# Optimization experiments

Measured on AMD Instinct MI355X. Metric: run time of the kernel, lower is better.

## Reference

```python
import jax, jax.numpy as jnp
import numpy as np

B, T, C, H = 8, 2048, 1024, 128

def setup_inputs() -> dict:
    key = jax.random.key(0)
    k1, k2, k3, k4 = jax.random.split(key, 4)
    x = jax.random.normal(k1, (B, T, C), dtype=jnp.float32)
    Wq = jax.random.normal(k2, (C, H), dtype=jnp.float32) * (C ** -0.5)
    Wk = jax.random.normal(k3, (C, H), dtype=jnp.float32) * (C ** -0.5)
    Wv = jax.random.normal(k4, (C, H), dtype=jnp.float32) * (C ** -0.5)
    return {"x": x, "Wq": Wq, "Wk": Wk, "Wv": Wv}

def reference(x, Wq, Wk, Wv):
    # x: [B,T,C]; projections (no bias)
    q = jnp.einsum('btc,ch->bth', x, Wq)
    k = jnp.einsum('btc,ch->bth', x, Wk)
    v = jnp.einsum('btc,ch->bth', x, Wv)
    # NOTE: original module has NO 1/sqrt(head_size) scaling
    scores = jnp.einsum('bth,bsh->bts', q, k)  # [B,T,T]
    t = scores.shape[1]
    causal = jnp.tril(jnp.ones((t, t), dtype=bool))
    scores = jnp.where(causal, scores, -jnp.inf)
    attn = jax.nn.softmax(scores, axis=-1)  # dropout is identity in eval
    out = jnp.einsum('bts,bsh->bth', attn, v)  # [B,T,H]
    return out
```

## Files before the change

kernel.cpp:

```cpp
#include <hip/hip_runtime.h>

typedef __bf16 bf16;
typedef _Float16 f16;
typedef f16 f16x4 __attribute__((ext_vector_type(4)));
typedef f16 f16x8 __attribute__((ext_vector_type(8)));
typedef float f32x4 __attribute__((ext_vector_type(4)));

#define MFMA_FP(a, b, c) __builtin_amdgcn_mfma_f32_16x16x32_f16((a), (b), (c), 0, 0, 0)

static constexpr int Bn = 8, T = 2048, C = 1024, H = 128;
static constexpr int M = Bn * T;

__global__ __launch_bounds__(256) void kwt(const float* __restrict__ Wq,
                                           const float* __restrict__ Wk,
                                           const float* __restrict__ Wv,
                                           f16* __restrict__ wt) {
  __shared__ float tl[32][33];
  const int w = blockIdx.z;
  const float* src = (w == 0) ? Wq : (w == 1) ? Wk : Wv;
  f16* dh = wt + (size_t)w * H * C;
  const int k0 = blockIdx.x * 32, n0 = blockIdx.y * 32;
  const int tx = threadIdx.x & 31, ty = threadIdx.x >> 5;
  for (int i = ty; i < 32; i += 8) tl[i][tx] = src[(size_t)(k0 + i) * H + n0 + tx];
  __syncthreads();
  for (int i = ty; i < 32; i += 8)
    dh[(size_t)(n0 + i) * C + k0 + tx] = (f16)tl[tx][i];
}

__global__ __launch_bounds__(256) void proj_kernel(const float* __restrict__ x,
                                                   const f16* __restrict__ wt,
                                                   f16* __restrict__ qo,
                                                   f16* __restrict__ ko,
                                                   f16* __restrict__ vt) {
  __shared__ __align__(16) f16 As[64 * 64];
  __shared__ __align__(16) f16 Bs[128 * 64];
  const int tid = threadIdx.x;
  const int lane = tid & 63, g = lane >> 4, r16 = lane & 15;
  const int wave = tid >> 6, wr = wave >> 1, wc = wave & 1;
  const int m0 = blockIdx.x * 64;
  const int which = blockIdx.y;
  const f16* wh = wt + (size_t)which * H * C;

  int arow[2], aoff[2], alds[2];
  int brow[4], boff[4], blds[4];
#pragma unroll
  for (int it = 0; it < 2; ++it) {
    const int c = it * 256 + tid, r = c >> 3, p = c & 7;
    arow[it] = r; aoff[it] = ((p ^ (r & 7)) << 3); alds[it] = r * 64 + p * 8;
  }
#pragma unroll
  for (int it = 0; it < 4; ++it) {
    const int c = it * 256 + tid, r = c >> 3, p = c & 7;
    brow[it] = r; boff[it] = ((p ^ (r & 7)) << 3); blds[it] = r * 64 + p * 8;
  }

  f32x4 ra[2][2]; f16x8 rb[4];
#pragma unroll
  for (int it = 0; it < 2; ++it) {
    ra[it][0] = *(const f32x4*)&x[(size_t)(m0 + arow[it]) * C + aoff[it]];
    ra[it][1] = *(const f32x4*)&x[(size_t)(m0 + arow[it]) * C + aoff[it] + 4];
  }
#pragma unroll
  for (int it = 0; it < 4; ++it)
    rb[it] = *(const f16x8*)&wh[(size_t)brow[it] * C + boff[it]];

  f32x4 acc[2][4] = {};

  for (int k0 = 0; k0 < C; k0 += 64) {
    __syncthreads();
#pragma unroll
    for (int it = 0; it < 2; ++it) {
      f16x8 av;
#pragma unroll
      for (int j = 0; j < 4; ++j) { av[j] = (f16)ra[it][0][j]; av[4 + j] = (f16)ra[it][1][j]; }
      *(f16x8*)&As[alds[it]] = av;
    }
#pragma unroll
    for (int it = 0; it < 4; ++it) *(f16x8*)&Bs[blds[it]] = rb[it];
    if (k0 + 64 < C) {
      const int kn = k0 + 64;
#pragma unroll
      for (int it = 0; it < 2; ++it) {
        ra[it][0] = *(const f32x4*)&x[(size_t)(m0 + arow[it]) * C + kn + aoff[it]];
        ra[it][1] = *(const f32x4*)&x[(size_t)(m0 + arow[it]) * C + kn + aoff[it] + 4];
      }
#pragma unroll
      for (int it = 0; it < 4; ++it)
        rb[it] = *(const f16x8*)&wh[(size_t)brow[it] * C + kn + boff[it]];
    }
    __syncthreads();
#pragma unroll
    for (int kb = 0; kb < 2; ++kb) {
      f16x8 af[2], bf[4];
#pragma unroll
      for (int mt = 0; mt < 2; ++mt) {
        const int r = wr * 32 + mt * 16 + r16;
        const int phys = (kb * 4 + g) ^ (r & 7);
        af[mt] = *(const f16x8*)&As[r * 64 + phys * 8];
      }
#pragma unroll
      for (int nt = 0; nt < 4; ++nt) {
        const int r = wc * 64 + nt * 16 + r16;
        const int phys = (kb * 4 + g) ^ (r & 7);
        bf[nt] = *(const f16x8*)&Bs[r * 64 + phys * 8];
      }
#pragma unroll
      for (int mt = 0; mt < 2; ++mt)
#pragma unroll
        for (int nt = 0; nt < 4; ++nt)
          acc[mt][nt] = MFMA_FP(af[mt], bf[nt], acc[mt][nt]);
    }
  }

  if (which < 2) {
    f16* dst = which ? ko : qo;
#pragma unroll
    for (int mt = 0; mt < 2; ++mt)
#pragma unroll
      for (int nt = 0; nt < 4; ++nt) {
        const int mb = m0 + wr * 32 + mt * 16 + g * 4;
        const int col = wc * 64 + nt * 16 + r16;
#pragma unroll
        for (int r = 0; r < 4; ++r)
          dst[(size_t)(mb + r) * H + col] = (f16)acc[mt][nt][r];
      }
  } else {
    const int b = m0 >> 11;
    const int tb0 = m0 & 2047;
    f16* vbase = vt + (size_t)b * H * T;
#pragma unroll
    for (int mt = 0; mt < 2; ++mt)
#pragma unroll
      for (int nt = 0; nt < 4; ++nt) {
        const int tib = tb0 + wr * 32 + mt * 16 + g * 4;
        const int h = wc * 64 + nt * 16 + r16;
        f16x4 pk;
#pragma unroll
        for (int r = 0; r < 4; ++r) pk[r] = (f16)acc[mt][nt][r];
        *(f16x4*)&vbase[(size_t)h * T + tib] = pk;
      }
  }
}

__global__ __launch_bounds__(256, 2) void attn_kernel(const f16* __restrict__ qp,
                                                      const f16* __restrict__ kp,
                                                      const f16* __restrict__ vp,
                                                      float* __restrict__ out,
                                                      f16* __restrict__ oS,
                                                      float* __restrict__ MLs) {
  __shared__ __align__(16) f16 KS[2][64 * 128];
  __shared__ __align__(16) f16 VS[2][128 * 64];
  __shared__ __align__(16) f16 Pl[4][16][72];

  const int tid = threadIdx.x, lane = tid & 63, wave = tid >> 6;
  const int g = lane >> 4, q15 = lane & 15;
  const int x7 = q15 & 7;
  const int bb = blockIdx.x;
  const int b = bb & 7;
  const int t2 = bb >> 3;
  const int qt = 31 - (t2 >> 1);
  const int par = t2 & 1;
  const int q0 = qt * 64;
  const int qrow = q0 + wave * 16 + q15;
  const int task = b * 32 + qt;

  const f16* qb = qp + (size_t)b * T * H;
  const f16* kb = kp + (size_t)b * T * H;
  const f16* vb = vp + (size_t)b * H * T;

  int koff[4], voff[4], lo[4];
#pragma unroll
  for (int i = 0; i < 4; ++i) {
    const int u = wave * 4 + i;
    const int rK = u * 4 + (lane >> 4);
    koff[i] = rK * H + (((lane & 15) ^ (rK & 7)) << 3);
    const int hV = u * 8 + (lane >> 3);
    voff[i] = hV * T + (((lane & 7) ^ (hV & 7)) << 3);
    lo[i] = u * 512 + lane * 8;
  }

  const int n = (qt >= par) ? ((qt - par) >> 1) + 1 : 0;

  f16x8 qf[4];
#pragma unroll
  for (int k4 = 0; k4 < 4; ++k4)
    qf[k4] = *(const f16x8*)&qb[(size_t)qrow * H + k4 * 32 + g * 8];

  f32x4 o[8] = {};
  float mrun = -1e30f, lrun = 0.f;

  f16x8 rk[4], rv[4];
#define LOADT(S0)                                                   \
  _Pragma("unroll")                                                 \
  for (int i = 0; i < 4; ++i) {                                     \
    rk[i] = *(const f16x8*)&kb[(size_t)(S0) * H + koff[i]];         \
    rv[i] = *(const f16x8*)&vb[(size_t)(S0) + voff[i]];             \
  }
#define WRITET(BUF)                                                 \
  _Pragma("unroll")                                                 \
  for (int i = 0; i < 4; ++i) {                                     \
    *(f16x8*)&KS[BUF][lo[i]] = rk[i];                               \
    *(f16x8*)&VS[BUF][lo[i]] = rv[i];                               \
  }

  if (n > 0) {
    LOADT(par * 64);
    WRITET(0);
    if (n > 1) LOADT(par * 64 + 128);

    for (int k = 0; k < n; ++k) {
      const int s0 = par * 64 + k * 128;
      const int cur = k & 1;
      __syncthreads();

      f32x4 sacc[4] = {};
#pragma unroll
      for (int mt = 0; mt < 4; ++mt) {
        const int row = mt * 16 + q15;
#pragma unroll
        for (int k4 = 0; k4 < 4; ++k4) {
          const int pch = (k4 * 4 + g) ^ (row & 7);
          const f16x8 kf = *(const f16x8*)&KS[cur][row * 128 + pch * 8];
          sacc[mt] = MFMA_FP(kf, qf[k4], sacc[mt]);
        }
      }
      if (k == n - 1) {
#pragma unroll
        for (int mt = 0; mt < 4; ++mt)
#pragma unroll
          for (int r = 0; r < 4; ++r)
            if (s0 + mt * 16 + g * 4 + r > qrow) sacc[mt][r] = -1e30f;
      }
      float tmax = -1e30f;
#pragma unroll
      for (int mt = 0; mt < 4; ++mt)
#pragma unroll
        for (int r = 0; r < 4; ++r) tmax = fmaxf(tmax, sacc[mt][r]);
      tmax = fmaxf(tmax, __shfl_xor(tmax, 16));
      tmax = fmaxf(tmax, __shfl_xor(tmax, 32));
      const float mnew = fmaxf(mrun, tmax);
      const float alpha = __expf(mrun - mnew);
      float lt = 0.f;
#pragma unroll
      for (int mt = 0; mt < 4; ++mt) {
        f16x4 pk;
#pragma unroll
        for (int r = 0; r < 4; ++r) {
          const float p = __expf(sacc[mt][r] - mnew);
          lt += p;
          pk[r] = (f16)p;
        }
        *(f16x4*)&Pl[wave][q15][mt * 16 + g * 4] = pk;
      }
      lt += __shfl_xor(lt, 16);
      lt += __shfl_xor(lt, 32);
      lrun = lrun * alpha + lt;
      mrun = mnew;
#pragma unroll
      for (int i = 0; i < 8; ++i) o[i] *= alpha;
      const f16x8 pf0 = *(const f16x8*)&Pl[wave][q15][g * 8];
      const f16x8 pf1 = *(const f16x8*)&Pl[wave][q15][32 + g * 8];
#pragma unroll
      for (int mt = 0; mt < 8; ++mt) {
        const int h = mt * 16 + q15;
        const f16x8 vf0 = *(const f16x8*)&VS[cur][h * 64 + ((g ^ x7) << 3)];
        o[mt] = MFMA_FP(vf0, pf0, o[mt]);
        const f16x8 vf1 = *(const f16x8*)&VS[cur][h * 64 + (((4 + g) ^ x7) << 3)];
        o[mt] = MFMA_FP(vf1, pf1, o[mt]);
      }

      if (k + 1 < n) {
        WRITET(cur ^ 1);
        if (k + 2 < n) LOADT(par * 64 + (k + 2) * 128);
      }
    }
  }
#undef LOADT
#undef WRITET

  const float inv = (lrun > 0.f) ? 1.0f / lrun : 0.f;
  if (lane < 16) {
    MLs[((size_t)(task * 2 + par) * 64 + wave * 16 + lane) * 2 + 0] = mrun;
    MLs[((size_t)(task * 2 + par) * 64 + wave * 16 + lane) * 2 + 1] = lrun;
  }
  if (par == 0) {
    float* ob = out + ((size_t)b * T + qrow) * H;
#pragma unroll
    for (int mt = 0; mt < 8; ++mt) {
      f32x4 pk;
#pragma unroll
      for (int r = 0; r < 4; ++r) pk[r] = o[mt][r] * inv;
      *(f32x4*)&ob[mt * 16 + g * 4] = pk;
    }
  } else {
    f16* sb = oS + ((size_t)task * 64 + wave * 16 + q15) * 128;
#pragma unroll
    for (int mt = 0; mt < 8; ++mt) {
      f16x4 pk;
#pragma unroll
      for (int r = 0; r < 4; ++r) pk[r] = (f16)(o[mt][r] * inv);
      *(f16x4*)&sb[mt * 16 + g * 4] = pk;
    }
  }
}

__global__ __launch_bounds__(256) void combine_kernel(float* __restrict__ out,
                                                      const f16* __restrict__ oS,
                                                      const float* __restrict__ MLs) {
  const int task = blockIdx.x;
  const int b = task >> 5, qt = task & 31;
  const int tid = threadIdx.x;
  const int row = tid >> 2;
  const int cb = (tid & 3) * 32;
  const float m0 = MLs[((size_t)(task * 2 + 0) * 64 + row) * 2 + 0];
  const float l0 = MLs[((size_t)(task * 2 + 0) * 64 + row) * 2 + 1];
  const float m1 = MLs[((size_t)(task * 2 + 1) * 64 + row) * 2 + 0];
  const float l1 = MLs[((size_t)(task * 2 + 1) * 64 + row) * 2 + 1];
  const float Mg = fmaxf(m0, m1);
  const float w0 = l0 * __expf(m0 - Mg);
  const float w1 = l1 * __expf(m1 - Mg);
  const float inv = 1.0f / (w0 + w1);
  float* orow = out + ((size_t)b * T + qt * 64 + row) * H + cb;
  const f16* srow = oS + ((size_t)task * 64 + row) * 128 + cb;
#pragma unroll
  for (int c = 0; c < 32; c += 8) {
    const f16x8 o1 = *(const f16x8*)&srow[c];
    f32x4 a0 = *(const f32x4*)&orow[c];
    f32x4 a1 = *(const f32x4*)&orow[c + 4];
    f32x4 r0, r1;
#pragma unroll
    for (int r = 0; r < 4; ++r) {
      r0[r] = (w0 * a0[r] + w1 * (float)o1[r]) * inv;
      r1[r] = (w0 * a1[r] + w1 * (float)o1[4 + r]) * inv;
    }
    *(f32x4*)&orow[c] = r0;
    *(f32x4*)&orow[c + 4] = r1;
  }
}

extern "C" void kernel_launch(void* const* d_in, const int* in_sizes, int n_in,
                              void* d_out, int out_size, void* d_ws, size_t ws_size,
                              hipStream_t stream) {
  const float* x  = (const float*)d_in[0];
  const float* Wq = (const float*)d_in[1];
  const float* Wk = (const float*)d_in[2];
  const float* Wv = (const float*)d_in[3];
  float* out = (float*)d_out;

  f16*  wt  = (f16*)d_ws;
  f16*  qf  = wt + (size_t)3 * H * C;
  f16*  kf  = qf + (size_t)M * H;
  f16*  vf  = kf + (size_t)M * H;
  f16*  oS  = vf + (size_t)M * H;
  float* MLs = (float*)(oS + (size_t)256 * 64 * 128);

  kwt<<<dim3(C / 32, H / 32, 3), 256, 0, stream>>>(Wq, Wk, Wv, wt);
  proj_kernel<<<dim3(M / 64, 3), 256, 0, stream>>>(x, wt, qf, kf, vf);
  attn_kernel<<<512, 256, 0, stream>>>(qf, kf, vf, out, oS, MLs);
  combine_kernel<<<256, 256, 0, stream>>>(out, oS, MLs);
}
```

Measured before the change: 67.52 us.

## Load projection tiles directly into LDS with global_load_lds and convert on read

The projection GEMM now uses global_load_lds so that x (kept as fp32) and the fp16 weight tiles are copied straight from global memory into shared memory, with an XOR swizzle applied at the source address. The fp32-to-fp16 conversion of x moves from the staging step to the point where fragments are read from LDS. This removes the VGPR staging round-trip and the register pressure that comes with it. In exchange, the x tile in LDS is twice as large. With a single buffer and the next load issued after compute, global loads no longer overlap the MFMA work.

```diff
diff --git a/kernel.cpp b/kernel.cpp
--- a/kernel.cpp
+++ b/kernel.cpp
@@ -10,6 +10,12 @@
 
 static constexpr int Bn = 8, T = 2048, C = 1024, H = 128;
 static constexpr int M = Bn * T;
+
+__device__ __forceinline__ void gll16(const void* g, void* l) {
+  __builtin_amdgcn_global_load_lds(
+      (const __attribute__((address_space(1))) unsigned int*)g,
+      (__attribute__((address_space(3))) unsigned int*)l, 16, 0, 0);
+}
 
 __global__ __launch_bounds__(256) void kwt(const float* __restrict__ Wq,
                                            const float* __restrict__ Wk,
@@ -32,8 +38,8 @@
                                                    f16* __restrict__ qo,
                                                    f16* __restrict__ ko,
                                                    f16* __restrict__ vt) {
-  __shared__ __align__(16) f16 As[64 * 64];
-  __shared__ __align__(16) f16 Bs[128 * 64];
+  __shared__ __align__(16) float As[64 * 64];
+  __shared__ __align__(16) f16  Bs[128 * 64];
   const int tid = threadIdx.x;
   const int lane = tid & 63, g = lane >> 4, r16 = lane & 15;
   const int wave = tid >> 6, wr = wave >> 1, wc = wave & 1;
@@ -41,62 +47,42 @@
   const int which = blockIdx.y;
   const f16* wh = wt + (size_t)which * H * C;
 
-  int arow[2], aoff[2], alds[2];
-  int brow[4], boff[4], blds[4];
-#pragma unroll
-  for (int it = 0; it < 2; ++it) {
-    const int c = it * 256 + tid, r = c >> 3, p = c & 7;
-    arow[it] = r; aoff[it] = ((p ^ (r & 7)) << 3); alds[it] = r * 64 + p * 8;
-  }
-#pragma unroll
-  for (int it = 0; it < 4; ++it) {
-    const int c = it * 256 + tid, r = c >> 3, p = c & 7;
-    brow[it] = r; boff[it] = ((p ^ (r & 7)) << 3); blds[it] = r * 64 + p * 8;
-  }
-
-  f32x4 ra[2][2]; f16x8 rb[4];
-#pragma unroll
-  for (int it = 0; it < 2; ++it) {
-    ra[it][0] = *(const f32x4*)&x[(size_t)(m0 + arow[it]) * C + aoff[it]];
-    ra[it][1] = *(const f32x4*)&x[(size_t)(m0 + arow[it]) * C + aoff[it] + 4];
-  }
-#pragma unroll
-  for (int it = 0; it < 4; ++it)
-    rb[it] = *(const f16x8*)&wh[(size_t)brow[it] * C + boff[it]];
+  int asrc[4], bsrc[4];
+  int aldu[4], bldu[4];
+#pragma unroll
+  for (int i = 0; i < 4; ++i) {
+    const int u = wave * 4 + i;
+    const int ra = u * 4 + (lane >> 4);
+    asrc[i] = (m0 + ra) * C + (((lane & 15) ^ (ra & 7)) << 2);
+    aldu[i] = u * 256;
+    const int rb = u * 8 + (lane >> 3);
+    bsrc[i] = rb * C + (((lane & 7) ^ (rb & 7)) << 3);
+    bldu[i] = u * 512;
+  }
 
   f32x4 acc[2][4] = {};
 
+#define ISSUE(K0)                                                  \
+  _Pragma("unroll")                                                \
+  for (int i = 0; i < 4; ++i) {                                    \
+    gll16(&x[asrc[i] + (K0)], &As[aldu[i]]);                       \
+    gll16(&wh[bsrc[i] + (K0)], &Bs[bldu[i]]);                      \
+  }
+
+  ISSUE(0);
   for (int k0 = 0; k0 < C; k0 += 64) {
     __syncthreads();
 #pragma unroll
-    for (int it = 0; it < 2; ++it) {
-      f16x8 av;
-#pragma unroll
-      for (int j = 0; j < 4; ++j) { av[j] = (f16)ra[it][0][j]; av[4 + j] = (f16)ra[it][1][j]; }
-      *(f16x8*)&As[alds[it]] = av;
-    }
-#pragma unroll
-    for (int it = 0; it < 4; ++it) *(f16x8*)&Bs[blds[it]] = rb[it];
-    if (k0 + 64 < C) {
-      const int kn = k0 + 64;
-#pragma unroll
-      for (int it = 0; it < 2; ++it) {
-        ra[it][0] = *(const f32x4*)&x[(size_t)(m0 + arow[it]) * C + kn + aoff[it]];
-        ra[it][1] = *(const f32x4*)&x[(size_t)(m0 + arow[it]) * C + kn + aoff[it] + 4];
-      }
-#pragma unroll
-      for (int it = 0; it < 4; ++it)
-        rb[it] = *(const f16x8*)&wh[(size_t)brow[it] * C + kn + boff[it]];
-    }
-    __syncthreads();
-#pragma unroll
     for (int kb = 0; kb < 2; ++kb) {
       f16x8 af[2], bf[4];
 #pragma unroll
       for (int mt = 0; mt < 2; ++mt) {
         const int r = wr * 32 + mt * 16 + r16;
-        const int phys = (kb * 4 + g) ^ (r & 7);
-        af[mt] = *(const f16x8*)&As[r * 64 + phys * 8];
+        const int s = r & 7;
+        const f32x4 a0 = *(const f32x4*)&As[r * 64 + (((kb * 8 + g * 2) ^ s) << 2)];
+        const f32x4 a1 = *(const f32x4*)&As[r * 64 + (((kb * 8 + g * 2 + 1) ^ s) << 2)];
+#pragma unroll
+        for (int j = 0; j < 4; ++j) { af[mt][j] = (f16)a0[j]; af[mt][4 + j] = (f16)a1[j]; }
       }
 #pragma unroll
       for (int nt = 0; nt < 4; ++nt) {
@@ -110,7 +96,10 @@
         for (int nt = 0; nt < 4; ++nt)
           acc[mt][nt] = MFMA_FP(af[mt], bf[nt], acc[mt][nt]);
     }
-  }
+    __syncthreads();
+    if (k0 + 64 < C) ISSUE(k0 + 64);
+  }
+#undef ISSUE
 
   if (which < 2) {
     f16* dst = which ? ko : qo;
```

After: 64.38 us. 1.05x faster.
